# Kernel tuning notes

Measured on AMD Instinct MI355X. Metric: run time of the kernel, lower is better.

Reference implementation:

```python
import jax, jax.numpy as jnp
import numpy as np

N, L, E, H, D = 4, 2048, 1024, 16, 64

def setup_inputs() -> dict:
    key = jax.random.key(0)
    ks = jax.random.split(key, 8)
    s = 1.0 / np.sqrt(E)
    return {
        "Q": jax.random.normal(ks[0], (N, L, E), jnp.float32),
        "K": jax.random.normal(ks[1], (N, L, E), jnp.float32),
        "V": jax.random.normal(ks[2], (N, L, E), jnp.float32),
        "Wq": jax.random.normal(ks[3], (H * D, E), jnp.float32) * s,
        "bq": jnp.zeros((H * D,), jnp.float32),
        "Wk": jax.random.normal(ks[4], (H * D, E), jnp.float32) * s,
        "bk": jnp.zeros((H * D,), jnp.float32),
        "Wv": jax.random.normal(ks[5], (H * D, E), jnp.float32) * s,
        "bv": jnp.zeros((H * D,), jnp.float32),
        "Wo": jax.random.normal(ks[6], (E, H * D), jnp.float32) * s,
        "bo": jnp.zeros((E,), jnp.float32),
    }

def reference(Q, K, V, Wq, bq, Wk, bk, Wv, bv, Wo, bo):
    n, lq, e = Q.shape
    lk = K.shape[1]
    # projections: Linear(x) = x @ W.T + b
    q = (Q @ Wq.T + bq).reshape(n, lq, H, D)
    k = (K @ Wk.T + bk).reshape(n, lk, H, D)
    v = (V @ Wv.T + bv).reshape(n, lk, H, D)
    # scores over key dim (original broadcasts Q*K and sums over d)
    scores = jnp.einsum('nqhd,nkhd->nqkh', q, k) / jnp.sqrt(jnp.float32(D))
    attn = jax.nn.softmax(scores, axis=2)  # softmax over key axis
    out = jnp.einsum('nqkh,nkhd->nqhd', attn, v)
    out = out.reshape(n, lq, H * D)
    return (out @ Wo.T + bo).reshape(n, lq, E)
```

## Files before the change

kernel.cpp:

```cpp
#include <hip/hip_runtime.h>
#include <cstdint>
#include <cstddef>


typedef __bf16 bf16x8 __attribute__((ext_vector_type(8)));
typedef __bf16 bf16x4 __attribute__((ext_vector_type(4)));
typedef __bf16 bf16x2 __attribute__((ext_vector_type(2)));
typedef float f32x4 __attribute__((ext_vector_type(4)));
typedef float f32x2 __attribute__((ext_vector_type(2)));
typedef unsigned int uint2v __attribute__((ext_vector_type(2)));
typedef unsigned int uint4v __attribute__((ext_vector_type(4)));

#define LOG2E_OVER_SQRTD 0.18033688011112042f

__device__ __forceinline__ unsigned short f2bf(float f) {
  unsigned int u = __builtin_bit_cast(unsigned int, f);
  u = (u + 0x7fffu + ((u >> 16) & 1u)) >> 16;
  return (unsigned short)u;
}

__device__ __forceinline__ unsigned int pk2(float a, float b) {
  f32x2 t = {a, b};
  bf16x2 h = __builtin_convertvector(t, bf16x2);
  return __builtin_bit_cast(unsigned int, h);
}

__device__ __forceinline__ void gl2lds16(const void* g, void* l) {
  __builtin_amdgcn_global_load_lds(
      (__attribute__((address_space(1))) unsigned int*)g,
      (__attribute__((address_space(3))) unsigned int*)l, 16, 0, 0);
}

struct CvtArgs {
  const float* src[4];
  unsigned short* dst[4];
};
__global__ __launch_bounds__(256) void cvt_multi_k(CvtArgs a) {
  const float* s = a.src[blockIdx.y];
  unsigned short* d = a.dst[blockIdx.y];
  size_t i = ((size_t)blockIdx.x * 256 + threadIdx.x) * 4;
  float4 v = *(const float4*)(s + i);
  ushort4 o;
  o.x = f2bf(v.x); o.y = f2bf(v.y); o.z = f2bf(v.z); o.w = f2bf(v.w);
  *(ushort4*)(d + i) = o;
}

struct GemmDesc {
  const unsigned short* A;
  const unsigned short* Bt;
  const float* bias;
  void* C;
  int N;
  int nbx_shift;
  float scale;
  int bias_row;
  int permc;
};
struct GemmPack3 {
  GemmDesc g[3];
};

template <bool OUT_F32>
__global__ __launch_bounds__(256, 2) void gemm_multi_k(GemmPack3 p) {
  __shared__ __attribute__((aligned(16))) unsigned short As[128 * 64];
  __shared__ __attribute__((aligned(16))) unsigned short Bs[128 * 64];
  const GemmDesc d = p.g[blockIdx.x >> 9];
  const int t = blockIdx.x & 511;
  const int bx = t & ((1 << d.nbx_shift) - 1);
  const int by = t >> d.nbx_shift;

  const int tid = threadIdx.x;
  const int lane = tid & 63, wave = tid >> 6;
  const int lr = lane & 15, lg = lane >> 4;
  const int rowBase = by * 128;
  const int colBase = bx * 128;
  const int wm = (wave & 1) * 64, wn = (wave >> 1) * 64;

  f32x4 acc[4][4] = {};

  const unsigned short* gA[4];
  const unsigned short* gB[4];
  unsigned short* lA[4];
  unsigned short* lB[4];
#pragma unroll
  for (int i = 0; i < 4; ++i) {
    int s = tid + i * 256;
    int row = s >> 3;
    int c = (s & 7) ^ (row & 7);
    gA[i] = d.A + (size_t)(rowBase + row) * 1024 + c * 8;
    gB[i] = d.Bt + (size_t)(colBase + row) * 1024 + c * 8;
    lA[i] = &As[s * 8];
    lB[i] = &Bs[s * 8];
  }

  for (int kt = 0; kt < 16; ++kt) {
    const int ko = kt * 64;
#pragma unroll
    for (int i = 0; i < 4; ++i) {
      gl2lds16(gA[i] + ko, lA[i]);
      gl2lds16(gB[i] + ko, lB[i]);
    }
    __syncthreads();

#pragma unroll
    for (int ks = 0; ks < 2; ++ks) {
      bf16x8 af[4], bfr[4];
#pragma unroll
      for (int mt = 0; mt < 4; ++mt) {
        int row = wm + mt * 16 + lr;
        int c = (ks * 4 + lg) ^ (row & 7);
        af[mt] = *(const bf16x8*)&As[row * 64 + c * 8];
      }
#pragma unroll
      for (int nt = 0; nt < 4; ++nt) {
        int row = wn + nt * 16 + lr;
        int c = (ks * 4 + lg) ^ (row & 7);
        bfr[nt] = *(const bf16x8*)&Bs[row * 64 + c * 8];
      }
#pragma unroll
      for (int mt = 0; mt < 4; ++mt)
#pragma unroll
        for (int nt = 0; nt < 4; ++nt)
          acc[mt][nt] = __builtin_amdgcn_mfma_f32_16x16x32_bf16(
              af[mt], bfr[nt], acc[mt][nt], 0, 0, 0);
    }
    __syncthreads();
  }

#pragma unroll
  for (int mt = 0; mt < 4; ++mt)
#pragma unroll
    for (int nt = 0; nt < 4; ++nt) {
      int col = colBase + wn + nt * 16 + lr;
      int colStore = d.permc ? (colBase + wn + lr * 4 + nt) : col;
      float bcol = d.bias_row ? 0.f : d.bias[col];
#pragma unroll
      for (int r = 0; r < 4; ++r) {
        int row = rowBase + wm + mt * 16 + lg * 4 + r;
        float b = d.bias_row ? d.bias[row] : bcol;
        float val = (acc[mt][nt][r] + b) * d.scale;
        size_t idx = (size_t)row * (size_t)d.N + (size_t)colStore;
        if (OUT_F32)
          ((float*)d.C)[idx] = val;
        else
          ((unsigned short*)d.C)[idx] = f2bf(val);
      }
    }
}

__global__ __launch_bounds__(256, 4) void attn_k(
    const unsigned short* __restrict__ qb,
    const unsigned short* __restrict__ kb,
    const unsigned short* __restrict__ vtb,
    unsigned short* __restrict__ aob) {
  __shared__ __attribute__((aligned(16))) unsigned short Ks[2 * 64 * 64];
  __shared__ __attribute__((aligned(16))) unsigned short Vts[2 * 64 * 64];

  const int tid = threadIdx.x;
  const int lane = tid & 63, wave = tid >> 6;
  const int lr = lane & 15, lg = lane >> 4;

  const int bid = blockIdx.x;
  const int xcd = bid & 7;
  const int idx = bid >> 3;
  const int qt = idx & 15;
  const int nh = (idx >> 4) * 8 + xcd;
  const int h = nh & 15, n = nh >> 4;
  const int q0 = qt * 128;

#pragma unroll
  for (int i = 0; i < 4; ++i) {
    int s = i * 256 + tid;
    int row = s >> 3;
    int c = (s & 7) ^ (row & 7);
    gl2lds16(qb + (((size_t)n * 2048 + q0 + row) << 10) + h * 64 + c * 8,
             &Ks[s * 8]);
  }
  __syncthreads();

  bf16x8 aq[2][2];
#pragma unroll
  for (int mt = 0; mt < 2; ++mt)
#pragma unroll
    for (int ks = 0; ks < 2; ++ks) {
      int row = wave * 32 + mt * 16 + lr;
      int c = (ks * 4 + lg) ^ (row & 7);
      aq[mt][ks] = *(const bf16x8*)&Ks[row * 64 + c * 8];
    }
  __syncthreads();

  const unsigned short* kg[2];
  const unsigned short* vg[2];
  int ldo[2];
#pragma unroll
  for (int i = 0; i < 2; ++i) {
    int s = i * 256 + tid;
    int row = s >> 3;
    int c = (s & 7) ^ (row & 7);
    kg[i] = kb + (((size_t)n * 2048 + row) << 10) + h * 64 + c * 8;
    vg[i] = vtb + (((size_t)(h * 64 + row)) << 13) + (size_t)n * 2048 + c * 8;
    ldo[i] = s * 8;
  }
#pragma unroll
  for (int i = 0; i < 2; ++i) {
    gl2lds16(kg[i], &Ks[ldo[i]]);
    gl2lds16(vg[i], &Vts[ldo[i]]);
    kg[i] += 64 * 1024;
    vg[i] += 64;
  }

  bf16x8 ones;
#pragma unroll
  for (int i = 0; i < 8; ++i) ones[i] = (__bf16)1.0f;

  f32x4 o_acc[2][4] = {};
  f32x4 o_sum[2] = {};

  for (int kt = 0; kt < 32; ++kt) {
    const int cb = (kt & 1) * 4096;
    const int nb = 4096 - cb;
    __syncthreads();

    if (kt < 31) {
#pragma unroll
      for (int i = 0; i < 2; ++i) {
        gl2lds16(kg[i], &Ks[nb + ldo[i]]);
        gl2lds16(vg[i], &Vts[nb + ldo[i]]);
        kg[i] += 64 * 1024;
        vg[i] += 64;
      }
    }

    f32x4 s_acc[2][4] = {};
#pragma unroll
    for (int ks = 0; ks < 2; ++ks)
#pragma unroll
      for (int nt = 0; nt < 4; ++nt) {
        int row = nt * 16 + lr;
        int c = (ks * 4 + lg) ^ (row & 7);
        bf16x8 kf = *(const bf16x8*)&Ks[cb + row * 64 + c * 8];
#pragma unroll
        for (int mt = 0; mt < 2; ++mt)
          s_acc[mt][nt] = __builtin_amdgcn_mfma_f32_16x16x32_bf16(
              kf, aq[mt][ks], s_acc[mt][nt], 0, 0, 0);
      }

    bf16x8 ap[2][2];
#pragma unroll
    for (int mt = 0; mt < 2; ++mt) {
#pragma unroll
      for (int ks = 0; ks < 2; ++ks) {
        float pe[2][4];
#pragma unroll
        for (int half = 0; half < 2; ++half) {
          int nt = ks * 2 + half;
#pragma unroll
          for (int r = 0; r < 4; ++r)
            pe[half][r] = __builtin_amdgcn_exp2f(s_acc[mt][nt][r]);
        }
        unsigned int x00 = pk2(pe[0][0], pe[0][1]);
        unsigned int x01 = pk2(pe[0][2], pe[0][3]);
        unsigned int x10 = pk2(pe[1][0], pe[1][1]);
        unsigned int x11 = pk2(pe[1][2], pe[1][3]);
        uint2v s0 = __builtin_amdgcn_permlane32_swap(x00, x10, false, false);
        uint2v t0 = __builtin_amdgcn_permlane16_swap(s0[0], s0[1], false, false);
        uint2v s1 = __builtin_amdgcn_permlane32_swap(x01, x11, false, false);
        uint2v t1 = __builtin_amdgcn_permlane16_swap(s1[0], s1[1], false, false);
        uint4v u;
        u[0] = t0[0];
        u[1] = t1[0];
        u[2] = t0[1];
        u[3] = t1[1];
        ap[mt][ks] = __builtin_bit_cast(bf16x8, u);
      }
    }

#pragma unroll
    for (int mt = 0; mt < 2; ++mt)
#pragma unroll
      for (int ks = 0; ks < 2; ++ks)
        o_sum[mt] = __builtin_amdgcn_mfma_f32_16x16x32_bf16(
            ap[mt][ks], ones, o_sum[mt], 0, 0, 0);

#pragma unroll
    for (int ks = 0; ks < 2; ++ks) {
      bf16x8 bv[4];
#pragma unroll
      for (int nt = 0; nt < 4; ++nt) {
        int row = nt * 16 + lr;
        int c = (ks * 4 + lg) ^ (row & 7);
        bv[nt] = *(const bf16x8*)&Vts[cb + row * 64 + c * 8];
      }
#pragma unroll
      for (int mt = 0; mt < 2; ++mt)
#pragma unroll
        for (int nt = 0; nt < 4; ++nt)
          o_acc[mt][nt] = __builtin_amdgcn_mfma_f32_16x16x32_bf16(
              ap[mt][ks], bv[nt], o_acc[mt][nt], 0, 0, 0);
    }
  }

#pragma unroll
  for (int mt = 0; mt < 2; ++mt) {
#pragma unroll
    for (int r = 0; r < 4; ++r) {
      float inv = 1.0f / o_sum[mt][r];
      int row_l = q0 + wave * 32 + mt * 16 + lg * 4 + r;
      size_t base = (((size_t)n * 2048 + row_l) << 10) + h * 64;
#pragma unroll
      for (int nt = 0; nt < 4; ++nt)
        aob[base + nt * 16 + lr] = f2bf(o_acc[mt][nt][r] * inv);
    }
  }
}

extern "C" void kernel_launch(void* const* d_in, const int* in_sizes, int n_in,
                              void* d_out, int out_size, void* d_ws,
                              size_t ws_size, hipStream_t stream) {
  const float* Q = (const float*)d_in[0];
  const float* K = (const float*)d_in[1];
  const float* V = (const float*)d_in[2];
  const float* Wq = (const float*)d_in[3];
  const float* bq = (const float*)d_in[4];
  const float* Wk = (const float*)d_in[5];
  const float* bk = (const float*)d_in[6];
  const float* Wv = (const float*)d_in[7];
  const float* bv = (const float*)d_in[8];
  const float* Wo = (const float*)d_in[9];
  const float* bo = (const float*)d_in[10];

  const size_t S = (size_t)8192 * 1024;
  const size_t W = (size_t)1024 * 1024;
  unsigned short* ws = (unsigned short*)d_ws;
  unsigned short* Qbf = ws;
  unsigned short* Kbf = ws + S;
  unsigned short* Vbf = ws + 2 * S;
  unsigned short* qbuf = ws + 3 * S;
  unsigned short* kbuf = ws + 4 * S;
  unsigned short* vtbuf = ws + 5 * S;
  unsigned short* Wqb = ws + 6 * S;
  unsigned short* Wkb = Wqb + W;
  unsigned short* Wvb = Wqb + 2 * W;
  unsigned short* Wob = Wqb + 3 * W;
  unsigned short* aob = Qbf;

  CvtArgs cx;
  cx.src[0] = Q; cx.dst[0] = Qbf;
  cx.src[1] = K; cx.dst[1] = Kbf;
  cx.src[2] = V; cx.dst[2] = Vbf;
  cx.src[3] = Q; cx.dst[3] = Qbf;
  cvt_multi_k<<<dim3(8192, 3), 256, 0, stream>>>(cx);

  CvtArgs cw;
  cw.src[0] = Wq; cw.dst[0] = Wqb;
  cw.src[1] = Wk; cw.dst[1] = Wkb;
  cw.src[2] = Wv; cw.dst[2] = Wvb;
  cw.src[3] = Wo; cw.dst[3] = Wob;
  cvt_multi_k<<<dim3(1024, 4), 256, 0, stream>>>(cw);

  GemmPack3 pp;
  pp.g[0] = {Qbf, Wqb, bq, qbuf, 1024, 3, LOG2E_OVER_SQRTD, 0, 0};
  pp.g[1] = {Kbf, Wkb, bk, kbuf, 1024, 3, 1.0f, 0, 0};
  pp.g[2] = {Wvb, Vbf, bv, vtbuf, 8192, 6, 1.0f, 1, 0};
  gemm_multi_k<false><<<1536, 256, 0, stream>>>(pp);

  attn_k<<<1024, 256, 0, stream>>>(qbuf, kbuf, vtbuf, aob);

  GemmPack3 po;
  po.g[0] = {aob, Wob, bo, d_out, 1024, 3, 1.0f, 0, 0};
  po.g[1] = po.g[0];
  po.g[2] = po.g[0];
  gemm_multi_k<true><<<512, 256, 0, stream>>>(po);
}
```

Measured before the change: 341.0 us.

## Merge conversion launches and restructure attention inner loop with hoisted LDS addressing

Folds the two fp32-to-bf16 conversion launches into one flat-grid kernel covering activations and weights, saving a kernel launch. In the attention kernel, LDS base addresses for K and V fragments are precomputed once, all fragments are loaded before the MFMA bursts, and the score accumulation starts from a zero constant instead of zero-initialised registers. It also raises wave priority around the MFMA sections with s_setprio and unrolls the key-tile loop by two. The goal is less address arithmetic and better overlap of LDS reads with matrix ops, at the cost of more live registers, which could reduce occupancy.

```diff
diff --git a/kernel.cpp b/kernel.cpp
--- a/kernel.cpp
+++ b/kernel.cpp
@@ -32,13 +32,23 @@
 }
 
 struct CvtArgs {
-  const float* src[4];
-  unsigned short* dst[4];
+  const float* src[7];
+  unsigned short* dst[7];
 };
-__global__ __launch_bounds__(256) void cvt_multi_k(CvtArgs a) {
-  const float* s = a.src[blockIdx.y];
-  unsigned short* d = a.dst[blockIdx.y];
-  size_t i = ((size_t)blockIdx.x * 256 + threadIdx.x) * 4;
+__global__ __launch_bounds__(256) void cvt_all_k(CvtArgs a) {
+  int bid = blockIdx.x;
+  int which, x;
+  if (bid < 24576) {
+    which = bid >> 13;
+    x = bid & 8191;
+  } else {
+    int r = bid - 24576;
+    which = 3 + (r >> 10);
+    x = r & 1023;
+  }
+  const float* s = a.src[which];
+  unsigned short* d = a.dst[which];
+  size_t i = ((size_t)x * 256 + threadIdx.x) * 4;
   float4 v = *(const float4*)(s + i);
   ushort4 o;
   o.x = f2bf(v.x); o.y = f2bf(v.y); o.z = f2bf(v.z); o.w = f2bf(v.w);
@@ -189,6 +199,13 @@
     }
   __syncthreads();
 
+  const int a0 = lr * 64 + ((lg ^ (lr & 7)) * 8);
+  const int a1 = lr * 64 + (((4 + lg) ^ (lr & 7)) * 8);
+  const unsigned short* Kb0 = &Ks[a0];
+  const unsigned short* Kb1 = &Ks[a1];
+  const unsigned short* Vb0 = &Vts[a0];
+  const unsigned short* Vb1 = &Vts[a1];
+
   const unsigned short* kg[2];
   const unsigned short* vg[2];
   int ldo[2];
@@ -212,10 +229,12 @@
   bf16x8 ones;
 #pragma unroll
   for (int i = 0; i < 8; ++i) ones[i] = (__bf16)1.0f;
+  const f32x4 fzero = {0.f, 0.f, 0.f, 0.f};
 
   f32x4 o_acc[2][4] = {};
   f32x4 o_sum[2] = {};
 
+#pragma unroll 2
   for (int kt = 0; kt < 32; ++kt) {
     const int cb = (kt & 1) * 4096;
     const int nb = 4096 - cb;
@@ -231,19 +250,24 @@
       }
     }
 
-    f32x4 s_acc[2][4] = {};
-#pragma unroll
-    for (int ks = 0; ks < 2; ++ks)
+    bf16x8 kf0[4], kf1[4];
+#pragma unroll
+    for (int nt = 0; nt < 4; ++nt) {
+      kf0[nt] = *(const bf16x8*)(Kb0 + cb + nt * 1024);
+      kf1[nt] = *(const bf16x8*)(Kb1 + cb + nt * 1024);
+    }
+    f32x4 s_acc[2][4];
+    __builtin_amdgcn_s_setprio(1);
+#pragma unroll
+    for (int mt = 0; mt < 2; ++mt)
 #pragma unroll
       for (int nt = 0; nt < 4; ++nt) {
-        int row = nt * 16 + lr;
-        int c = (ks * 4 + lg) ^ (row & 7);
-        bf16x8 kf = *(const bf16x8*)&Ks[cb + row * 64 + c * 8];
-#pragma unroll
-        for (int mt = 0; mt < 2; ++mt)
-          s_acc[mt][nt] = __builtin_amdgcn_mfma_f32_16x16x32_bf16(
-              kf, aq[mt][ks], s_acc[mt][nt], 0, 0, 0);
-      }
+        f32x4 t0 = __builtin_amdgcn_mfma_f32_16x16x32_bf16(
+            kf0[nt], aq[mt][0], fzero, 0, 0, 0);
+        s_acc[mt][nt] = __builtin_amdgcn_mfma_f32_16x16x32_bf16(
+            kf1[nt], aq[mt][1], t0, 0, 0, 0);
+      }
+    __builtin_amdgcn_s_setprio(0);
 
     bf16x8 ap[2][2];
 #pragma unroll
@@ -275,29 +299,28 @@
       }
     }
 
-#pragma unroll
-    for (int mt = 0; mt < 2; ++mt)
-#pragma unroll
-      for (int ks = 0; ks < 2; ++ks)
-        o_sum[mt] = __builtin_amdgcn_mfma_f32_16x16x32_bf16(
-            ap[mt][ks], ones, o_sum[mt], 0, 0, 0);
-
-#pragma unroll
-    for (int ks = 0; ks < 2; ++ks) {
-      bf16x8 bv[4];
+    bf16x8 bv0[4], bv1[4];
+#pragma unroll
+    for (int nt = 0; nt < 4; ++nt) {
+      bv0[nt] = *(const bf16x8*)(Vb0 + cb + nt * 1024);
+      bv1[nt] = *(const bf16x8*)(Vb1 + cb + nt * 1024);
+    }
+    __builtin_amdgcn_s_setprio(1);
+#pragma unroll
+    for (int mt = 0; mt < 2; ++mt) {
+      o_sum[mt] = __builtin_amdgcn_mfma_f32_16x16x32_bf16(
+          ap[mt][0], ones, o_sum[mt], 0, 0, 0);
+      o_sum[mt] = __builtin_amdgcn_mfma_f32_16x16x32_bf16(
+          ap[mt][1], ones, o_sum[mt], 0, 0, 0);
 #pragma unroll
       for (int nt = 0; nt < 4; ++nt) {
-        int row = nt * 16 + lr;
-        int c = (ks * 4 + lg) ^ (row & 7);
-        bv[nt] = *(const bf16x8*)&Vts[cb + row * 64 + c * 8];
-      }
-#pragma unroll
-      for (int mt = 0; mt < 2; ++mt)
-#pragma unroll
-        for (int nt = 0; nt < 4; ++nt)
-          o_acc[mt][nt] = __builtin_amdgcn_mfma_f32_16x16x32_bf16(
-              ap[mt][ks], bv[nt], o_acc[mt][nt], 0, 0, 0);
-    }
+        o_acc[mt][nt] = __builtin_amdgcn_mfma_f32_16x16x32_bf16(
+            ap[mt][0], bv0[nt], o_acc[mt][nt], 0, 0, 0);
+        o_acc[mt][nt] = __builtin_amdgcn_mfma_f32_16x16x32_bf16(
+            ap[mt][1], bv1[nt], o_acc[mt][nt], 0, 0, 0);
+      }
+    }
+    __builtin_amdgcn_s_setprio(0);
   }
 
 #pragma unroll
@@ -344,19 +367,15 @@
   unsigned short* Wob = Wqb + 3 * W;
   unsigned short* aob = Qbf;
 
-  CvtArgs cx;
-  cx.src[0] = Q; cx.dst[0] = Qbf;
-  cx.src[1] = K; cx.dst[1] = Kbf;
-  cx.src[2] = V; cx.dst[2] = Vbf;
-  cx.src[3] = Q; cx.dst[3] = Qbf;
-  cvt_multi_k<<<dim3(8192, 3), 256, 0, stream>>>(cx);
-
-  CvtArgs cw;
-  cw.src[0] = Wq; cw.dst[0] = Wqb;
-  cw.src[1] = Wk; cw.dst[1] = Wkb;
-  cw.src[2] = Wv; cw.dst[2] = Wvb;
-  cw.src[3] = Wo; cw.dst[3] = Wob;
-  cvt_multi_k<<<dim3(1024, 4), 256, 0, stream>>>(cw);
+  CvtArgs cv;
+  cv.src[0] = Q;  cv.dst[0] = Qbf;
+  cv.src[1] = K;  cv.dst[1] = Kbf;
+  cv.src[2] = V;  cv.dst[2] = Vbf;
+  cv.src[3] = Wq; cv.dst[3] = Wqb;
+  cv.src[4] = Wk; cv.dst[4] = Wkb;
+  cv.src[5] = Wv; cv.dst[5] = Wvb;
+  cv.src[6] = Wo; cv.dst[6] = Wob;
+  cvt_all_k<<<28672, 256, 0, stream>>>(cv);
 
   GemmPack3 pp;
   pp.g[0] = {Qbf, Wqb, bq, qbuf, 1024, 3, LOG2E_OVER_SQRTD, 0, 0};
```

Measured after the change: 337.8 us. No clear change (-0.9%).
